# Kernel tuning notes

Measured on AMD Instinct MI355X. Metric: run time of the kernel, lower is better.

The kernel has to match this reference:

```python
import jax, jax.numpy as jnp
import numpy as np

B, S, D = 2, 2048, 1024
H, DK = 16, 64


def setup_inputs() -> dict:
    key = jax.random.key(0)
    ks = jax.random.split(key, 10)
    scale = D ** -0.5
    x = jax.random.normal(ks[0], (B, S, D), dtype=jnp.float32)
    mask = jax.random.randint(ks[1], (B, S), 0, 2) > 0  # True = masked positions
    Wq = jax.random.normal(ks[2], (D, H * DK), dtype=jnp.float32) * scale
    Wk = jax.random.normal(ks[3], (D, H * DK), dtype=jnp.float32) * scale
    Wv = jax.random.normal(ks[4], (D, H * DK), dtype=jnp.float32) * scale
    Wo = jax.random.normal(ks[5], (H * DK, D), dtype=jnp.float32) * scale
    bq = jnp.zeros((H * DK,), jnp.float32)
    bk = jnp.zeros((H * DK,), jnp.float32)
    bv = jnp.zeros((H * DK,), jnp.float32)
    bo = jnp.zeros((D,), jnp.float32)
    return {"x": x, "mask": mask, "Wq": Wq, "bq": bq, "Wk": Wk, "bk": bk,
            "Wv": Wv, "bv": bv, "Wo": Wo, "bo": bo}


def reference(x, mask, Wq, bq, Wk, bk, Wv, bv, Wo, bo):
    b, s, _ = x.shape
    # Linear + activation (dropout is identity at eval)
    q = jax.nn.relu(x @ Wq + bq).reshape(b, s, H, DK)
    k = jax.nn.relu(x @ Wk + bk).reshape(b, s, H, DK)
    v = jax.nn.relu(x @ Wv + bv).reshape(b, s, H, DK)
    # scores: [B, H, Sq, Sk]
    attn = jnp.einsum("bqhd,bkhd->bhqk", q, k) * (DK ** -0.5)
    # NOTE: original uses masked_fill(mask, 1e-9) BEFORE softmax (not -inf)
    attn = jnp.where(mask[:, None, None, :], jnp.float32(1e-9), attn)
    attn = jax.nn.softmax(attn, axis=-1)
    out = jnp.einsum("bhqk,bkhd->bqhd", attn, v).reshape(b, s, H * DK)
    return jax.nn.relu(out @ Wo + bo)
```

## Files before the change

kernel.cpp:

```cpp
#include <hip/hip_runtime.h>
#include <stdint.h>

typedef __attribute__((ext_vector_type(8))) short short8;
typedef __attribute__((ext_vector_type(4))) short short4b;
typedef __attribute__((ext_vector_type(4))) float f32x4;
typedef __attribute__((ext_vector_type(4))) unsigned short ushort4_t;

#define MFMA16(a, b, c) __builtin_amdgcn_mfma_f32_16x16x32_bf16((a), (b), (c), 0, 0, 0)

#if defined(__HIP_DEVICE_COMPILE__)
  #if __has_builtin(__builtin_amdgcn_mfma_f32_16x16x16bf16_1k)
    #define MFMA16K16(a, b, c) __builtin_amdgcn_mfma_f32_16x16x16bf16_1k((a), (b), (c), 0, 0, 0)
  #else
    #define MFMA16K16(a, b, c) __builtin_amdgcn_mfma_f32_16x16x16_bf16((a), (b), (c), 0, 0, 0)
  #endif
  #if __has_builtin(__builtin_amdgcn_exp2f)
    #define EXP2(x) __builtin_amdgcn_exp2f(x)
  #else
    #define EXP2(x) exp2f(x)
  #endif
#else
  #define MFMA16K16(a, b, c) (c)
  #define EXP2(x) exp2f(x)
#endif

#define SCL_F (0.125f * 1.44269504f)

__device__ __forceinline__ float b2f(unsigned short u) {
    union { unsigned u; float f; } c; c.u = ((unsigned)u) << 16; return c.f;
}
__device__ __forceinline__ unsigned short f2b(float f) {
    union { float f; unsigned u; } c; c.f = f;
    unsigned r = c.u + 0x7FFF + ((c.u >> 16) & 1);
    return (unsigned short)(r >> 16);
}
__device__ __forceinline__ unsigned f_as_u(float f) {
    union { float f; unsigned u; } c; c.f = f; return c.u;
}

__device__ __forceinline__ void g2lds16(const unsigned short* g, unsigned lds_byte_off) {
    __builtin_amdgcn_global_load_lds(
        (const __attribute__((address_space(1))) void*)(uintptr_t)g,
        (__attribute__((address_space(3))) void*)(uintptr_t)lds_byte_off,
        16, 0, 0);
}

__global__ void detect_dtype(const unsigned short* __restrict__ x, int* __restrict__ flag) {
    __shared__ int cnt;
    if (threadIdx.x == 0) cnt = 0;
    __syncthreads();
    int insane = 0;
    #pragma unroll
    for (int j = 0; j < 4; ++j) {
        unsigned short u = x[threadIdx.x * 4 + j];
        int e = (u >> 7) & 0xFF;
        if ((e >= 1 && e <= 90) || e >= 165) insane++;
    }
    atomicAdd(&cnt, insane);
    __syncthreads();
    if (threadIdx.x == 0) *flag = (cnt > 128) ? 1 : 0;
}

__global__ __launch_bounds__(256) void convtrans_k(const void* __restrict__ s0, const void* __restrict__ s1,
                                                   const void* __restrict__ s2, const void* __restrict__ s3,
                                                   const void* __restrict__ b0, const void* __restrict__ b1,
                                                   const void* __restrict__ b2, const void* __restrict__ b3s,
                                                   const void* __restrict__ xsrc,
                                                   unsigned short* __restrict__ xdst,
                                                   unsigned short* __restrict__ dstBase,
                                                   unsigned short* __restrict__ dstB3,
                                                   unsigned short* __restrict__ dstBo,
                                                   const int* __restrict__ flag) {
    const int z = blockIdx.z;
    if (z >= 5) {
        if (!*flag) return;
        const int slice = z - 5;
        const size_t i0 = (size_t)slice * 524288 + (blockIdx.y * 16 + blockIdx.x) * 2048 + threadIdx.x * 8;
        const float* s = (const float*)xsrc;
        float4 f0 = *(const float4*)&s[i0];
        float4 f1 = *(const float4*)&s[i0 + 4];
        unsigned short* t = &xdst[i0];
        t[0] = f2b(f0.x); t[1] = f2b(f0.y); t[2] = f2b(f0.z); t[3] = f2b(f0.w);
        t[4] = f2b(f1.x); t[5] = f2b(f1.y); t[6] = f2b(f1.z); t[7] = f2b(f1.w);
        return;
    }
    if (z == 4) {
        if (blockIdx.y != 0 || blockIdx.x >= 4) return;
        const int w = blockIdx.x;
        const void* src = (w == 0) ? b0 : (w == 1) ? b1 : (w == 2) ? b2 : b3s;
        const float bscl = (w == 0) ? SCL_F : 1.0f;
        #pragma unroll
        for (int j = 0; j < 4; ++j) {
            const int i = threadIdx.x * 4 + j;
            float fv = (*flag) ? ((const float*)src)[i] : b2f(((const unsigned short*)src)[i]);
            unsigned short v = f2b(fv * bscl);
            if (w < 3) dstB3[w * 1024 + i] = v;
            else dstBo[i] = v;
        }
        return;
    }
    __shared__ __align__(16) unsigned short tile[64 * 72];
    const void* src = (z == 0) ? s0 : (z == 1) ? s1 : (z == 2) ? s2 : s3;
    unsigned short* dst = dstBase + (size_t)z * 1024 * 1024;
    const float wscl = (z == 0) ? SCL_F : 1.0f;
    const int tid = threadIdx.x;
    const int r0 = blockIdx.y * 64, c0 = blockIdx.x * 64;
    const int rb = tid >> 3, c = (tid & 7) * 8;
    if (*flag) {
        const float* s = (const float*)src;
        #pragma unroll
        for (int it = 0; it < 2; ++it) {
            int rr = it * 32 + rb;
            float4 f0 = *(const float4*)&s[(size_t)(r0 + rr) * 1024 + c0 + c];
            float4 f1 = *(const float4*)&s[(size_t)(r0 + rr) * 1024 + c0 + c + 4];
            unsigned short* t = &tile[rr * 72 + c];
            t[0] = f2b(f0.x * wscl); t[1] = f2b(f0.y * wscl); t[2] = f2b(f0.z * wscl); t[3] = f2b(f0.w * wscl);
            t[4] = f2b(f1.x * wscl); t[5] = f2b(f1.y * wscl); t[6] = f2b(f1.z * wscl); t[7] = f2b(f1.w * wscl);
        }
    } else if (z == 0) {
        const unsigned short* s = (const unsigned short*)src;
        #pragma unroll
        for (int it = 0; it < 2; ++it) {
            int rr = it * 32 + rb;
            union { short8 v; unsigned short u[8]; } in;
            in.v = *(const short8*)&s[(size_t)(r0 + rr) * 1024 + c0 + c];
            unsigned short* t = &tile[rr * 72 + c];
            #pragma unroll
            for (int j = 0; j < 8; ++j) t[j] = f2b(b2f(in.u[j]) * SCL_F);
        }
    } else {
        const unsigned short* s = (const unsigned short*)src;
        #pragma unroll
        for (int it = 0; it < 2; ++it) {
            int rr = it * 32 + rb;
            *(short8*)&tile[rr * 72 + c] = *(const short8*)&s[(size_t)(r0 + rr) * 1024 + c0 + c];
        }
    }
    __syncthreads();
    #pragma unroll
    for (int it = 0; it < 2; ++it) {
        int n = it * 32 + rb, k8 = c;
        union { short8 s; unsigned short u[8]; } tmp;
        #pragma unroll
        for (int j = 0; j < 8; ++j) tmp.u[j] = tile[(k8 + j) * 72 + n];
        *(short8*)&dst[(size_t)(c0 + n) * 1024 + r0 + k8] = tmp.s;
    }
}

__global__ __launch_bounds__(256) void mask_k(unsigned short* __restrict__ qkv,
                                              const int* __restrict__ mask) {
    const int row = blockIdx.x * 2 + (threadIdx.x >> 7);
    const int col = (threadIdx.x & 127) * 8;
    if (mask[row]) {
        const short8 z = {0, 0, 0, 0, 0, 0, 0, 0};
        *(short8*)&qkv[(size_t)row * 3072 + 1024 + col] = z;
    }
}

__global__ __launch_bounds__(256) void gemm_bias_relu(const unsigned short* __restrict__ A,
                                                      const void* __restrict__ Araw,
                                                      const unsigned short* __restrict__ BT,
                                                      const unsigned short* __restrict__ bias,
                                                      void* __restrict__ C,
                                                      unsigned short* __restrict__ VtG,
                                                      const int* __restrict__ flag,
                                                      int M, int N, int K, int mode) {
    __shared__ __align__(16) unsigned short As[3][128 * 32];
    __shared__ __align__(16) unsigned short Bs[3][128 * 32];
    const int tid = threadIdx.x;
    const int wave = tid >> 6, lane = tid & 63;
    const int quad = lane >> 4, l16 = lane & 15;
    const int wm = wave >> 1, wn = wave & 1;
    const int m0 = blockIdx.y * 128, n0 = blockIdx.x * 128;

    const unsigned short* Ause = (Araw != nullptr && *flag == 0) ? (const unsigned short*)Araw : A;

    f32x4 acc[4][4];
    #pragma unroll
    for (int i = 0; i < 4; i++)
        #pragma unroll
        for (int j = 0; j < 4; j++) acc[i][j] = (f32x4){0.f, 0.f, 0.f, 0.f};

    const int srow = wave * 32 + (lane >> 2);
    const int sc8  = (lane & 3) * 8;
    const unsigned short* gA0 = Ause + (size_t)(m0 + srow) * K + sc8;
    const unsigned short* gA1 = gA0 + (size_t)16 * K;
    const unsigned short* gB0 = BT + (size_t)(n0 + srow) * K + sc8;
    const unsigned short* gB1 = gB0 + (size_t)16 * K;

    unsigned lA0 = (unsigned)(uintptr_t)&As[0][0] + wave * 2048;
    unsigned lA1 = (unsigned)(uintptr_t)&As[1][0] + wave * 2048;
    unsigned lA2 = (unsigned)(uintptr_t)&As[2][0] + wave * 2048;
    unsigned lB0 = (unsigned)(uintptr_t)&Bs[0][0] + wave * 2048;
    unsigned lB1 = (unsigned)(uintptr_t)&Bs[1][0] + wave * 2048;
    unsigned lB2 = (unsigned)(uintptr_t)&Bs[2][0] + wave * 2048;
    const unsigned short* pA0 = &As[0][0];
    const unsigned short* pA1 = &As[1][0];
    const unsigned short* pA2 = &As[2][0];
    const unsigned short* pB0 = &Bs[0][0];
    const unsigned short* pB1 = &Bs[1][0];
    const unsigned short* pB2 = &Bs[2][0];

    g2lds16(gA0, lA0); g2lds16(gA1, lA0 + 1024);
    g2lds16(gB0, lB0); g2lds16(gB1, lB0 + 1024);
    if (32 < K) {
        g2lds16(gA0 + 32, lA1); g2lds16(gA1 + 32, lA1 + 1024);
        g2lds16(gB0 + 32, lB1); g2lds16(gB1 + 32, lB1 + 1024);
    }
    if (64 < K) {
        g2lds16(gA0 + 64, lA2); g2lds16(gA1 + 64, lA2 + 1024);
        g2lds16(gB0 + 64, lB2); g2lds16(gB1 + 64, lB2 + 1024);
    }

    for (int k0 = 0; k0 < K; k0 += 32) {
        if (k0 + 64 < K)       asm volatile("s_waitcnt vmcnt(8)" ::: "memory");
        else if (k0 + 32 < K)  asm volatile("s_waitcnt vmcnt(4)" ::: "memory");
        else                   asm volatile("s_waitcnt vmcnt(0)" ::: "memory");
        __builtin_amdgcn_s_barrier();

        short8 af[4], bf[4];
        #pragma unroll
        for (int i = 0; i < 4; i++) af[i] = *(const short8*)&pA0[(wm * 64 + i * 16 + l16) * 32 + quad * 8];
        #pragma unroll
        for (int j = 0; j < 4; j++) bf[j] = *(const short8*)&pB0[(wn * 64 + j * 16 + l16) * 32 + quad * 8];
        #pragma unroll
        for (int i = 0; i < 4; i++)
            #pragma unroll
            for (int j = 0; j < 4; j++)
                acc[i][j] = MFMA16(af[i], bf[j], acc[i][j]);

        __builtin_amdgcn_s_barrier();

        if (k0 + 96 < K) {
            g2lds16(gA0 + k0 + 96, lA0); g2lds16(gA1 + k0 + 96, lA0 + 1024);
            g2lds16(gB0 + k0 + 96, lB0); g2lds16(gB1 + k0 + 96, lB0 + 1024);
        }
        unsigned tu;
        tu = lA0; lA0 = lA1; lA1 = lA2; lA2 = tu;
        tu = lB0; lB0 = lB1; lB1 = lB2; lB2 = tu;
        const unsigned short* tp;
        tp = pA0; pA0 = pA1; pA1 = pA2; pA2 = tp;
        tp = pB0; pB0 = pB1; pB1 = pB2; pB2 = tp;
    }

    if (mode == 2 && n0 >= 2048) {
        #pragma unroll
        for (int j = 0; j < 4; j++) {
            const int col = n0 + wn * 64 + j * 16 + l16;
            const int h  = (col - 2048) >> 6;
            const int dk = (col - 2048) & 63;
            const float bj = b2f(bias[col]);
            #pragma unroll
            for (int i = 0; i < 4; i++) {
                const int rowb = m0 + wm * 64 + i * 16 + quad * 4;
                const int bb = rowb >> 11;
                const int s0 = rowb & 2047;
                ushort4_t w;
                #pragma unroll
                for (int r = 0; r < 4; r++) {
                    float v = acc[i][j][r] + bj;
                    v = v > 0.f ? v : 0.f;
                    w[r] = f2b(v);
                }
                *(ushort4_t*)&VtG[(size_t)((bb * 16 + h) * 64 + dk) * 2048 + s0] = w;
            }
        }
    } else {
        const int f32out = (mode == 1) && (*flag != 0);
        #pragma unroll
        for (int j = 0; j < 4; j++) {
            const int col = n0 + wn * 64 + j * 16 + l16;
            const float bj = b2f(bias[col]);
            #pragma unroll
            for (int i = 0; i < 4; i++) {
                const int rowb = m0 + wm * 64 + i * 16 + quad * 4;
                #pragma unroll
                for (int r = 0; r < 4; r++) {
                    float v = acc[i][j][r] + bj;
                    v = v > 0.f ? v : 0.f;
                    if (f32out) ((float*)C)[(size_t)(rowb + r) * N + col] = v;
                    else ((unsigned short*)C)[(size_t)(rowb + r) * N + col] = f2b(v);
                }
            }
        }
    }
}

__global__ __launch_bounds__(256) void gemm64_bias_relu(const unsigned short* __restrict__ A,
                                                        const unsigned short* __restrict__ BT,
                                                        const unsigned short* __restrict__ bias,
                                                        void* __restrict__ C,
                                                        const int* __restrict__ flag,
                                                        int N, int K) {
    __shared__ __align__(16) unsigned short As[3][64 * 32];
    __shared__ __align__(16) unsigned short Bs[3][128 * 32];
    const int tid = threadIdx.x;
    const int wave = tid >> 6, lane = tid & 63;
    const int quad = lane >> 4, l16 = lane & 15;
    const int wm = wave >> 1, wn = wave & 1;
    const int m0 = blockIdx.y * 64, n0 = blockIdx.x * 128;

    f32x4 acc[2][4];
    #pragma unroll
    for (int i = 0; i < 2; i++)
        #pragma unroll
        for (int j = 0; j < 4; j++) acc[i][j] = (f32x4){0.f, 0.f, 0.f, 0.f};

    const int arow = tid >> 2, ac8 = (tid & 3) * 8;
    const unsigned short* gA0 = A + (size_t)(m0 + arow) * K + ac8;
    const int brow = wave * 32 + (lane >> 2), bc8 = (lane & 3) * 8;
    const unsigned short* gB0 = BT + (size_t)(n0 + brow) * K + bc8;
    const unsigned short* gB1 = gB0 + (size_t)16 * K;

    unsigned lA0 = (unsigned)(uintptr_t)&As[0][0] + wave * 1024;
    unsigned lA1 = (unsigned)(uintptr_t)&As[1][0] + wave * 1024;
    unsigned lA2 = (unsigned)(uintptr_t)&As[2][0] + wave * 1024;
    unsigned lB0 = (unsigned)(uintptr_t)&Bs[0][0] + wave * 2048;
    unsigned lB1 = (unsigned)(uintptr_t)&Bs[1][0] + wave * 2048;
    unsigned lB2 = (unsigned)(uintptr_t)&Bs[2][0] + wave * 2048;
    const unsigned short* pA0 = &As[0][0];
    const unsigned short* pA1 = &As[1][0];
    const unsigned short* pA2 = &As[2][0];
    const unsigned short* pB0 = &Bs[0][0];
    const unsigned short* pB1 = &Bs[1][0];
    const unsigned short* pB2 = &Bs[2][0];

    g2lds16(gA0, lA0);
    g2lds16(gB0, lB0); g2lds16(gB1, lB0 + 1024);
    if (32 < K) {
        g2lds16(gA0 + 32, lA1);
        g2lds16(gB0 + 32, lB1); g2lds16(gB1 + 32, lB1 + 1024);
    }
    if (64 < K) {
        g2lds16(gA0 + 64, lA2);
        g2lds16(gB0 + 64, lB2); g2lds16(gB1 + 64, lB2 + 1024);
    }

    for (int k0 = 0; k0 < K; k0 += 32) {
        if (k0 + 64 < K)       asm volatile("s_waitcnt vmcnt(6)" ::: "memory");
        else if (k0 + 32 < K)  asm volatile("s_waitcnt vmcnt(3)" ::: "memory");
        else                   asm volatile("s_waitcnt vmcnt(0)" ::: "memory");
        __builtin_amdgcn_s_barrier();

        short8 af[2], bf[4];
        #pragma unroll
        for (int i = 0; i < 2; i++) af[i] = *(const short8*)&pA0[(wm * 32 + i * 16 + l16) * 32 + quad * 8];
        #pragma unroll
        for (int j = 0; j < 4; j++) bf[j] = *(const short8*)&pB0[(wn * 64 + j * 16 + l16) * 32 + quad * 8];
        #pragma unroll
        for (int i = 0; i < 2; i++)
            #pragma unroll
            for (int j = 0; j < 4; j++)
                acc[i][j] = MFMA16(af[i], bf[j], acc[i][j]);

        __builtin_amdgcn_s_barrier();

        if (k0 + 96 < K) {
            g2lds16(gA0 + k0 + 96, lA0);
            g2lds16(gB0 + k0 + 96, lB0); g2lds16(gB1 + k0 + 96, lB0 + 1024);
        }
        unsigned tu;
        tu = lA0; lA0 = lA1; lA1 = lA2; lA2 = tu;
        tu = lB0; lB0 = lB1; lB1 = lB2; lB2 = tu;
        const unsigned short* tp;
        tp = pA0; pA0 = pA1; pA1 = pA2; pA2 = tp;
        tp = pB0; pB0 = pB1; pB1 = pB2; pB2 = tp;
    }

    const int f32out = (*flag != 0);
    #pragma unroll
    for (int j = 0; j < 4; j++) {
        const int col = n0 + wn * 64 + j * 16 + l16;
        const float bj = b2f(bias[col]);
        #pragma unroll
        for (int i = 0; i < 2; i++) {
            const int rowb = m0 + wm * 32 + i * 16 + quad * 4;
            #pragma unroll
            for (int r = 0; r < 4; r++) {
                float v = acc[i][j][r] + bj;
                v = v > 0.f ? v : 0.f;
                if (f32out) ((float*)C)[(size_t)(rowb + r) * N + col] = v;
                else ((unsigned short*)C)[(size_t)(rowb + r) * N + col] = f2b(v);
            }
        }
    }
}

#define ATTN_TILE(Kbuf, Vbuf)                                                            \
    do {                                                                                 \
        __builtin_amdgcn_s_setprio(1);                                                   \
        f32x4 sA[4], sB[4];                                                              \
        _Pragma("unroll")                                                                \
        for (int t = 0; t < 4; ++t) {                                                    \
            const short8 kb0 = *(const short8*)&(Kbuf)[(((t * 16 + l16) * 64) + quad * 8) ^ rx];       \
            const short8 kb1 = *(const short8*)&(Kbuf)[(((t * 16 + l16) * 64) + 32 + quad * 8) ^ rx];  \
            f32x4 z = (f32x4){0.f, 0.f, 0.f, 0.f};                                       \
            sA[t] = MFMA16(kb1, qa1, MFMA16(kb0, qa0, z));                               \
            sB[t] = MFMA16(kb1, qb1, MFMA16(kb0, qb0, z));                               \
        }                                                                                \
        short4b vb[4][4];                                                                \
        _Pragma("unroll")                                                                \
        for (int t = 0; t < 4; ++t)                                                      \
            _Pragma("unroll")                                                            \
            for (int n = 0; n < 4; ++n)                                                  \
                vb[t][n] = *(const short4b*)&(Vbuf)[(((n * 16 + l16) * 64) + t * 16 + quad * 4) ^ rx]; \
        _Pragma("unroll")                                                                \
        for (int t = 0; t < 4; ++t) {                                                    \
            float pA[4], pB[4];                                                          \
            _Pragma("unroll")                                                            \
            for (int r = 0; r < 4; ++r) {                                                \
                pA[r] = EXP2(sA[t][r]);                                                  \
                pB[r] = EXP2(sB[t][r]);                                                  \
            }                                                                            \
            union { unsigned u[2]; short4b s; } fa, fb;                                  \
            fa.u[0] = __builtin_amdgcn_perm(f_as_u(pA[1]), f_as_u(pA[0]), 0x07060302u);  \
            fa.u[1] = __builtin_amdgcn_perm(f_as_u(pA[3]), f_as_u(pA[2]), 0x07060302u);  \
            fb.u[0] = __builtin_amdgcn_perm(f_as_u(pB[1]), f_as_u(pB[0]), 0x07060302u);  \
            fb.u[1] = __builtin_amdgcn_perm(f_as_u(pB[3]), f_as_u(pB[2]), 0x07060302u);  \
            _Pragma("unroll")                                                            \
            for (int n = 0; n < 4; ++n) {                                                \
                oA[n] = MFMA16K16(fa.s, vb[t][n], oA[n]);                                \
                oB[n] = MFMA16K16(fb.s, vb[t][n], oB[n]);                                \
            }                                                                            \
            sumA = MFMA16K16(fa.s, ones, sumA);                                          \
            sumB = MFMA16K16(fb.s, ones, sumB);                                          \
        }                                                                                \
        __builtin_amdgcn_s_setprio(0);                                                   \
    } while (0)

__global__ __launch_bounds__(256) void attn_kernel(const unsigned short* __restrict__ qkv,
                                                   const unsigned short* __restrict__ VtG,
                                                   unsigned short* __restrict__ out) {
    __shared__ __align__(16) unsigned short Ks[2][64 * 64];
    __shared__ __align__(16) unsigned short Vs[2][64 * 64];

    const int l = blockIdx.y * 16 + blockIdx.x;
    const int v = (l & 7) * 64 + (l >> 3);
    const int qt = v & 15, bh = v >> 4;
    const int b = bh >> 4, h = bh & 15;
    const int tid = threadIdx.x, wave = tid >> 6, lane = tid & 63;
    const int quad = lane >> 4, l16 = lane & 15;

    const int qrowA = qt * 128 + wave * 16 + l16;
    const unsigned short* qpA = qkv + (size_t)(b * 2048 + qrowA) * 3072 + h * 64;
    const unsigned short* qpB = qpA + (size_t)64 * 3072;
    const short8 qa0 = *(const short8*)(qpA + quad * 8);
    const short8 qa1 = *(const short8*)(qpA + 32 + quad * 8);
    const short8 qb0 = *(const short8*)(qpB + quad * 8);
    const short8 qb1 = *(const short8*)(qpB + 32 + quad * 8);

    f32x4 oA[4], oB[4], sumA, sumB;
    #pragma unroll
    for (int n = 0; n < 4; n++) { oA[n] = (f32x4){0.f,0.f,0.f,0.f}; oB[n] = (f32x4){0.f,0.f,0.f,0.f}; }
    sumA = (f32x4){0.f,0.f,0.f,0.f};
    sumB = (f32x4){0.f,0.f,0.f,0.f};

    const short4b ones = { (short)0x3F80, (short)0x3F80, (short)0x3F80, (short)0x3F80 };

    const int srow = tid >> 2;
    const int scol = (tid & 3) * 16;
    const int sxor = (srow & 7) << 3;
    const unsigned short* kg = qkv + (size_t)(b * 2048 + srow) * 3072 + 1024 + h * 64 + scol;
    const unsigned short* vg = VtG + (size_t)(bh * 64 + srow) * 2048 + scol;
    const size_t kstep = (size_t)64 * 3072;
    const int sidx0 = (srow * 64 + scol) ^ sxor;
    const int sidx1 = (srow * 64 + scol + 8) ^ sxor;
    unsigned short* wK0a = &Ks[0][sidx0];  unsigned short* wK1a = &Ks[0][sidx1];
    unsigned short* wV0a = &Vs[0][sidx0];  unsigned short* wV1a = &Vs[0][sidx1];
    unsigned short* wK0b = &Ks[1][sidx0];  unsigned short* wK1b = &Ks[1][sidx1];
    unsigned short* wV0b = &Vs[1][sidx0];  unsigned short* wV1b = &Vs[1][sidx1];

    const int rx = (l16 & 7) << 3;

    short8 rkA0 = *(const short8*)(kg);
    short8 rkA1 = *(const short8*)(kg + 8);
    short8 rvA0 = *(const short8*)(vg);
    short8 rvA1 = *(const short8*)(vg + 8);
    *(short8*)wK0a = rkA0;  *(short8*)wK1a = rkA1;
    *(short8*)wV0a = rvA0;  *(short8*)wV1a = rvA1;
    short8 rkB0 = *(const short8*)(kg + kstep);
    short8 rkB1 = *(const short8*)(kg + kstep + 8);
    short8 rvB0 = *(const short8*)(vg + 64);
    short8 rvB1 = *(const short8*)(vg + 64 + 8);
    __syncthreads();

    for (int kt = 0; kt < 32; kt += 2) {
        *(short8*)wK0b = rkB0;  *(short8*)wK1b = rkB1;
        *(short8*)wV0b = rvB0;  *(short8*)wV1b = rvB1;
        if (kt + 2 < 32) {
            rkA0 = *(const short8*)(kg + (kt + 2) * kstep);
            rkA1 = *(const short8*)(kg + (kt + 2) * kstep + 8);
            rvA0 = *(const short8*)(vg + (kt + 2) * 64);
            rvA1 = *(const short8*)(vg + (kt + 2) * 64 + 8);
        }
        ATTN_TILE(Ks[0], Vs[0]);
        __syncthreads();

        if (kt + 2 < 32) {
            *(short8*)wK0a = rkA0;  *(short8*)wK1a = rkA1;
            *(short8*)wV0a = rvA0;  *(short8*)wV1a = rvA1;
        }
        if (kt + 3 < 32) {
            rkB0 = *(const short8*)(kg + (kt + 3) * kstep);
            rkB1 = *(const short8*)(kg + (kt + 3) * kstep + 8);
            rvB0 = *(const short8*)(vg + (kt + 3) * 64);
            rvB1 = *(const short8*)(vg + (kt + 3) * 64 + 8);
        }
        ATTN_TILE(Ks[1], Vs[1]);
        __syncthreads();
    }

    float invA[4], invB[4];
    #pragma unroll
    for (int r = 0; r < 4; ++r) { invA[r] = 1.0f / sumA[r]; invB[r] = 1.0f / sumB[r]; }
    #pragma unroll
    for (int n = 0; n < 4; n++)
        #pragma unroll
        for (int r = 0; r < 4; r++) {
            const int row = qt * 128 + wave * 16 + quad * 4 + r;
            out[(size_t)(b * 2048 + row) * 1024 + h * 64 + n * 16 + l16] = f2b(oA[n][r] * invA[r]);
            out[(size_t)(b * 2048 + row + 64) * 1024 + h * 64 + n * 16 + l16] = f2b(oB[n][r] * invB[r]);
        }
}

extern "C" void kernel_launch(void* const* d_in, const int* in_sizes, int n_in,
                              void* d_out, int out_size, void* d_ws, size_t ws_size,
                              hipStream_t stream) {
    const void* x  = d_in[0];
    const int*  mk = (const int*)d_in[1];
    const void* Wq = d_in[2]; const void* bq = d_in[3];
    const void* Wk = d_in[4]; const void* bk = d_in[5];
    const void* Wv = d_in[6]; const void* bv = d_in[7];
    const void* Wo = d_in[8]; const void* bo = d_in[9];

    char* wsb = (char*)d_ws;
    int* flag = (int*)wsb;
    unsigned short* W0 = (unsigned short*)(wsb + 64);

    const size_t M1 = 1024u * 1024u;
    const size_t M4 = 4096u * 1024u;
    unsigned short* xb  = W0;
    unsigned short* WT  = xb + M4;
    unsigned short* WoT = WT + 3 * M1;
    unsigned short* b3  = WoT + M1;
    unsigned short* bob = b3 + 4096;
    unsigned short* qkv = bob + 1024;
    unsigned short* VtG = qkv + (size_t)4096 * 3072;
    unsigned short* abf = xb;

    detect_dtype<<<1, 256, 0, stream>>>((const unsigned short*)x, flag);

    convtrans_k<<<dim3(16, 16, 13), 256, 0, stream>>>(Wq, Wk, Wv, Wo, bq, bk, bv, bo,
                                                      x, xb, WT, b3, bob, flag);

    gemm_bias_relu<<<dim3(24, 32), 256, 0, stream>>>(xb, x, WT, b3, qkv, VtG, flag,
                                                     4096, 3072, 1024, 2);
    mask_k<<<2048, 256, 0, stream>>>(qkv, mk);
    attn_kernel<<<dim3(16, 32), 256, 0, stream>>>(qkv, VtG, abf);
    gemm64_bias_relu<<<dim3(8, 64), 256, 0, stream>>>(abf, WoT, bob, d_out, flag, 1024, 1024);
}
```

Before: 198.3 us.

## Fuse key masking into QKV GEMM and stage epilogue through LDS for coalesced stores

Specializes the QKV GEMM into gemm_qkv, which stages the bias+ReLU output tile in shared memory and then writes it with 16-byte coalesced row stores. The V-transpose output is written the same way. Key masking is applied during these stores, so the separate mask_k launch and its extra pass over the K slice are removed. The x fp32-to-bf16 conversion now uses one vector store instead of eight scalar stores. The epilogue adds a __syncthreads and reuses the pipeline LDS buffers, which makes the correctness of buffer reuse depend on the main loop's final barrier.

```diff
diff --git a/kernel.cpp b/kernel.cpp
--- a/kernel.cpp
+++ b/kernel.cpp
@@ -4,7 +4,6 @@
 typedef __attribute__((ext_vector_type(8))) short short8;
 typedef __attribute__((ext_vector_type(4))) short short4b;
 typedef __attribute__((ext_vector_type(4))) float f32x4;
-typedef __attribute__((ext_vector_type(4))) unsigned short ushort4_t;
 
 #define MFMA16(a, b, c) __builtin_amdgcn_mfma_f32_16x16x32_bf16((a), (b), (c), 0, 0, 0)
 
@@ -79,9 +78,10 @@
         const float* s = (const float*)xsrc;
         float4 f0 = *(const float4*)&s[i0];
         float4 f1 = *(const float4*)&s[i0 + 4];
-        unsigned short* t = &xdst[i0];
-        t[0] = f2b(f0.x); t[1] = f2b(f0.y); t[2] = f2b(f0.z); t[3] = f2b(f0.w);
-        t[4] = f2b(f1.x); t[5] = f2b(f1.y); t[6] = f2b(f1.z); t[7] = f2b(f1.w);
+        union { short8 v; unsigned short u[8]; } o;
+        o.u[0] = f2b(f0.x); o.u[1] = f2b(f0.y); o.u[2] = f2b(f0.z); o.u[3] = f2b(f0.w);
+        o.u[4] = f2b(f1.x); o.u[5] = f2b(f1.y); o.u[6] = f2b(f1.z); o.u[7] = f2b(f1.w);
+        *(short8*)&xdst[i0] = o.v;
         return;
     }
     if (z == 4) {
@@ -147,26 +147,16 @@
     }
 }
 
-__global__ __launch_bounds__(256) void mask_k(unsigned short* __restrict__ qkv,
-                                              const int* __restrict__ mask) {
-    const int row = blockIdx.x * 2 + (threadIdx.x >> 7);
-    const int col = (threadIdx.x & 127) * 8;
-    if (mask[row]) {
-        const short8 z = {0, 0, 0, 0, 0, 0, 0, 0};
-        *(short8*)&qkv[(size_t)row * 3072 + 1024 + col] = z;
-    }
-}
-
-__global__ __launch_bounds__(256) void gemm_bias_relu(const unsigned short* __restrict__ A,
-                                                      const void* __restrict__ Araw,
-                                                      const unsigned short* __restrict__ BT,
-                                                      const unsigned short* __restrict__ bias,
-                                                      void* __restrict__ C,
-                                                      unsigned short* __restrict__ VtG,
-                                                      const int* __restrict__ flag,
-                                                      int M, int N, int K, int mode) {
-    __shared__ __align__(16) unsigned short As[3][128 * 32];
-    __shared__ __align__(16) unsigned short Bs[3][128 * 32];
+__global__ __launch_bounds__(256) void gemm_qkv(const unsigned short* __restrict__ A,
+                                                const void* __restrict__ Araw,
+                                                const unsigned short* __restrict__ BT,
+                                                const unsigned short* __restrict__ bias,
+                                                unsigned short* __restrict__ qkv,
+                                                unsigned short* __restrict__ VtG,
+                                                const int* __restrict__ mask,
+                                                const int* __restrict__ flag,
+                                                int K) {
+    __shared__ __align__(16) unsigned short smem[24576];
     const int tid = threadIdx.x;
     const int wave = tid >> 6, lane = tid & 63;
     const int quad = lane >> 4, l16 = lane & 15;
@@ -188,18 +178,20 @@
     const unsigned short* gB0 = BT + (size_t)(n0 + srow) * K + sc8;
     const unsigned short* gB1 = gB0 + (size_t)16 * K;
 
-    unsigned lA0 = (unsigned)(uintptr_t)&As[0][0] + wave * 2048;
-    unsigned lA1 = (unsigned)(uintptr_t)&As[1][0] + wave * 2048;
-    unsigned lA2 = (unsigned)(uintptr_t)&As[2][0] + wave * 2048;
-    unsigned lB0 = (unsigned)(uintptr_t)&Bs[0][0] + wave * 2048;
-    unsigned lB1 = (unsigned)(uintptr_t)&Bs[1][0] + wave * 2048;
-    unsigned lB2 = (unsigned)(uintptr_t)&Bs[2][0] + wave * 2048;
-    const unsigned short* pA0 = &As[0][0];
-    const unsigned short* pA1 = &As[1][0];
-    const unsigned short* pA2 = &As[2][0];
-    const unsigned short* pB0 = &Bs[0][0];
-    const unsigned short* pB1 = &Bs[1][0];
-    const unsigned short* pB2 = &Bs[2][0];
+    const unsigned sA = (unsigned)(uintptr_t)&smem[0];
+    const unsigned sB = sA + 24576;
+    unsigned lA0 = sA + wave * 2048;
+    unsigned lA1 = sA + 8192 + wave * 2048;
+    unsigned lA2 = sA + 16384 + wave * 2048;
+    unsigned lB0 = sB + wave * 2048;
+    unsigned lB1 = sB + 8192 + wave * 2048;
+    unsigned lB2 = sB + 16384 + wave * 2048;
+    const unsigned short* pA0 = &smem[0];
+    const unsigned short* pA1 = &smem[4096];
+    const unsigned short* pA2 = &smem[8192];
+    const unsigned short* pB0 = &smem[12288];
+    const unsigned short* pB1 = &smem[16384];
+    const unsigned short* pB2 = &smem[20480];
 
     g2lds16(gA0, lA0); g2lds16(gA1, lA0 + 1024);
     g2lds16(gB0, lB0); g2lds16(gB1, lB0 + 1024);
@@ -243,46 +235,58 @@
         tp = pB0; pB0 = pB1; pB1 = pB2; pB2 = tp;
     }
 
-    if (mode == 2 && n0 >= 2048) {
+    unsigned short* epi = &smem[0];
+    if (n0 >= 2048) {
         #pragma unroll
         for (int j = 0; j < 4; j++) {
-            const int col = n0 + wn * 64 + j * 16 + l16;
-            const int h  = (col - 2048) >> 6;
-            const int dk = (col - 2048) & 63;
-            const float bj = b2f(bias[col]);
+            const int cl = wn * 64 + j * 16 + l16;
+            const float bj = b2f(bias[n0 + cl]);
             #pragma unroll
             for (int i = 0; i < 4; i++) {
-                const int rowb = m0 + wm * 64 + i * 16 + quad * 4;
-                const int bb = rowb >> 11;
-                const int s0 = rowb & 2047;
-                ushort4_t w;
+                const int rl = wm * 64 + i * 16 + quad * 4;
                 #pragma unroll
                 for (int r = 0; r < 4; r++) {
                     float v = acc[i][j][r] + bj;
                     v = v > 0.f ? v : 0.f;
-                    w[r] = f2b(v);
+                    epi[cl * 132 + rl + r] = f2b(v);
                 }
-                *(ushort4_t*)&VtG[(size_t)((bb * 16 + h) * 64 + dk) * 2048 + s0] = w;
             }
         }
+        __syncthreads();
+        const int cl = tid >> 1, half = (tid & 1) * 64;
+        const int colg = n0 + cl;
+        const int h  = (colg - 2048) >> 6;
+        const int dk = (colg - 2048) & 63;
+        const int bb = m0 >> 11;
+        unsigned short* dst = &VtG[((size_t)(bb * 16 + h) * 64 + dk) * 2048 + (m0 & 2047) + half];
+        const unsigned short* src = &epi[cl * 132 + half];
+        #pragma unroll
+        for (int k = 0; k < 8; k++) *(short8*)&dst[k * 8] = *(const short8*)&src[k * 8];
     } else {
-        const int f32out = (mode == 1) && (*flag != 0);
         #pragma unroll
         for (int j = 0; j < 4; j++) {
-            const int col = n0 + wn * 64 + j * 16 + l16;
-            const float bj = b2f(bias[col]);
+            const int cl = wn * 64 + j * 16 + l16;
+            const float bj = b2f(bias[n0 + cl]);
             #pragma unroll
             for (int i = 0; i < 4; i++) {
-                const int rowb = m0 + wm * 64 + i * 16 + quad * 4;
+                const int rl = wm * 64 + i * 16 + quad * 4;
                 #pragma unroll
                 for (int r = 0; r < 4; r++) {
                     float v = acc[i][j][r] + bj;
                     v = v > 0.f ? v : 0.f;
-                    if (f32out) ((float*)C)[(size_t)(rowb + r) * N + col] = v;
-                    else ((unsigned short*)C)[(size_t)(rowb + r) * N + col] = f2b(v);
+                    epi[(rl + r) * 132 + cl] = f2b(v);
                 }
             }
         }
+        __syncthreads();
+        const int row = tid >> 1, half = (tid & 1) * 64;
+        const int rowg = m0 + row;
+        const int mz = (n0 >= 1024) && mask[rowg];
+        unsigned short* dst = &qkv[(size_t)rowg * 3072 + n0 + half];
+        const unsigned short* src = &epi[row * 132 + half];
+        const short8 zero = {0, 0, 0, 0, 0, 0, 0, 0};
+        #pragma unroll
+        for (int k = 0; k < 8; k++) *(short8*)&dst[k * 8] = mz ? zero : *(const short8*)&src[k * 8];
     }
 }
 
@@ -553,9 +557,7 @@
     convtrans_k<<<dim3(16, 16, 13), 256, 0, stream>>>(Wq, Wk, Wv, Wo, bq, bk, bv, bo,
                                                       x, xb, WT, b3, bob, flag);
 
-    gemm_bias_relu<<<dim3(24, 32), 256, 0, stream>>>(xb, x, WT, b3, qkv, VtG, flag,
-                                                     4096, 3072, 1024, 2);
-    mask_k<<<2048, 256, 0, stream>>>(qkv, mk);
+    gemm_qkv<<<dim3(24, 32), 256, 0, stream>>>(xb, x, WT, b3, qkv, VtG, mk, flag, 1024);
     attn_kernel<<<dim3(16, 32), 256, 0, stream>>>(qkv, VtG, abf);
     gemm64_bias_relu<<<dim3(8, 64), 256, 0, stream>>>(abf, WoT, bob, d_out, flag, 1024, 1024);
 }
```

Result: no change. 202.2 us (+1.9%).
